# Performance work log

Measured on AMD Instinct MI355X. Metric: run time of the kernel, lower is better.

Reference implementation:

```python
import jax, jax.numpy as jnp
import numpy as np

N = 50000
E = 1600000
F_IN = 4
F_OUT = 32
PERIODS = 12


def setup_inputs() -> dict:
    key = jax.random.key(0)
    ks = jax.random.split(key, 18)
    s_in = 1.0 / np.sqrt(F_IN)
    s_cat = 1.0 / np.sqrt(2 * F_OUT)
    s_out = 1.0 / np.sqrt(F_OUT)
    inp = {
        'x': jax.random.normal(ks[0], (N, F_IN, PERIODS), dtype=jnp.float32),
        'edge_index': jax.random.randint(ks[1], (2, E), 0, N, dtype=jnp.int32),
        'attention': jax.random.uniform(ks[2], (PERIODS,), dtype=jnp.float32),
        # GRU update gate z: GCNConv weight/bias + Linear(2*F_OUT -> F_OUT)
        'Wz': jax.random.normal(ks[3], (F_IN, F_OUT), jnp.float32) * s_in,
        'bz': jnp.zeros((F_OUT,), jnp.float32),
        'Lz': jax.random.normal(ks[4], (2 * F_OUT, F_OUT), jnp.float32) * s_cat,
        'lz': jnp.zeros((F_OUT,), jnp.float32),
        # reset gate r
        'Wr': jax.random.normal(ks[5], (F_IN, F_OUT), jnp.float32) * s_in,
        'br': jnp.zeros((F_OUT,), jnp.float32),
        'Lr': jax.random.normal(ks[6], (2 * F_OUT, F_OUT), jnp.float32) * s_cat,
        'lr': jnp.zeros((F_OUT,), jnp.float32),
        # candidate h
        'Wh': jax.random.normal(ks[7], (F_IN, F_OUT), jnp.float32) * s_in,
        'bh': jnp.zeros((F_OUT,), jnp.float32),
        'Lh': jax.random.normal(ks[8], (2 * F_OUT, F_OUT), jnp.float32) * s_cat,
        'lh': jnp.zeros((F_OUT,), jnp.float32),
        # outer Linear(32 -> periods)
        'Wo': jax.random.normal(ks[9], (F_OUT, PERIODS), jnp.float32) * s_out,
        'bo': jnp.zeros((PERIODS,), jnp.float32),
    }
    return inp


def reference(x, edge_index, attention, Wz, bz, Lz, lz, Wr, br, Lr, lr, Wh, bh, Lh, lh, Wo, bo):
    n = x.shape[0]
    # gcn_norm: add self loops, symmetric D^-1/2 (A+I) D^-1/2
    loop = jnp.arange(n, dtype=edge_index.dtype)
    row = jnp.concatenate([edge_index[0], loop])  # source
    col = jnp.concatenate([edge_index[1], loop])  # target
    w = jnp.ones(row.shape[0], dtype=x.dtype)
    deg = jax.ops.segment_sum(w, col, num_segments=n)
    dinv = jnp.where(deg > 0, jax.lax.rsqrt(deg), 0.0)
    norm = dinv[row] * dinv[col]  # [E+N]

    def conv(xt, W, b):
        h = xt @ W                                   # [N, F_OUT]
        msg = h[row] * norm[:, None]                 # gather + scale
        return jax.ops.segment_sum(msg, col, num_segments=n) + b

    H0 = jnp.zeros((n, F_OUT), dtype=x.dtype)  # A3TGCN passes H=None each period

    def tgcn(xt):
        Z = jax.nn.sigmoid(jnp.concatenate([conv(xt, Wz, bz), H0], axis=1) @ Lz + lz)
        R = jax.nn.sigmoid(jnp.concatenate([conv(xt, Wr, br), H0], axis=1) @ Lr + lr)
        Ht = jnp.tanh(jnp.concatenate([conv(xt, Wh, bh), H0 * R], axis=1) @ Lh + lh)
        return Z * H0 + (1.0 - Z) * Ht

    Hs = jax.vmap(tgcn)(jnp.moveaxis(x, 2, 0))       # [T, N, F_OUT]
    probs = jax.nn.softmax(attention)
    H = jnp.einsum('tnc,t->nc', Hs, probs)           # attention-weighted sum over periods
    return jax.nn.relu(H) @ Wo + bo                  # [N, PERIODS]
```

## Files before the change

kernel.cpp:

```cpp
#include <hip/hip_runtime.h>
#include <hip/hip_fp16.h>
#include <math.h>

#define CHUNK 6144
#define CAPG  10240
#define GNODES 21

union U2H { uint2 u; __half2 h[2]; };

__global__ void k_pre(const float* __restrict__ Wz, const float* __restrict__ Lz, const float* __restrict__ lz,
                      const float* __restrict__ Wh, const float* __restrict__ Lh, const float* __restrict__ lh,
                      const float* __restrict__ bz, const float* __restrict__ bh,
                      const float* __restrict__ att,
                      float* __restrict__ AzT, float* __restrict__ AhT,
                      float* __restrict__ bzp, float* __restrict__ bhp, float* __restrict__ probs,
                      int* __restrict__ gcur) {
  int t = threadIdx.x;
  gcur[t] = 0;
  if (t < 128) {
    int f = t >> 2, k = t & 3;
    float s = 0.f, s2 = 0.f;
    for (int j = 0; j < 32; ++j) {
      s  = fmaf(Wz[k * 32 + j], Lz[j * 32 + f], s);
      s2 = fmaf(Wh[k * 32 + j], Lh[j * 32 + f], s2);
    }
    AzT[t] = s; AhT[t] = s2;
  }
  if (t >= 128 && t < 160) {
    int f = t - 128;
    float s = lz[f], s2 = lh[f];
    for (int j = 0; j < 32; ++j) {
      s  = fmaf(bz[j], Lz[j * 32 + f], s);
      s2 = fmaf(bh[j], Lh[j * 32 + f], s2);
    }
    bzp[f] = s; bhp[f] = s2;
  }
  if (t == 160) {
    float m = att[0];
    for (int i = 1; i < 12; ++i) m = fmaxf(m, att[i]);
    float e[12]; float s = 0.f;
    for (int i = 0; i < 12; ++i) { e[i] = __expf(att[i] - m); s += e[i]; }
    for (int i = 0; i < 12; ++i) probs[i] = e[i] / s;
  }
}

__global__ __launch_bounds__(1024) void k_part(const int* __restrict__ row, const int* __restrict__ col,
                                               int E, int nbkt,
                                               int* __restrict__ gcur, unsigned* __restrict__ part) {
  __shared__ unsigned spak[CHUNK];
  __shared__ unsigned char sbkt[CHUNK];
  __shared__ unsigned char slc[CHUNK];
  __shared__ int hist[256], sscan[256], scur[256], gbase[256];
  int t = threadIdx.x;
  int base = blockIdx.x * CHUNK;
  int cnt = E - base; if (cnt > CHUNK) cnt = CHUNK;
  if (t < 256) hist[t] = 0;
  __syncthreads();
  for (int i = t; i < cnt; i += 1024) {
    int c = col[base + i];
    int b = c >> 8;
    sbkt[i] = (unsigned char)b;
    slc[i]  = (unsigned char)(c & 255);
    atomicAdd(&hist[b], 1);
  }
  __syncthreads();
  int v = 0;
  if (t < 256) { v = hist[t]; sscan[t] = v; }
  __syncthreads();
  for (int off = 1; off < 256; off <<= 1) {
    int a = 0;
    if (t < 256 && t >= off) a = sscan[t - off];
    __syncthreads();
    if (t < 256) sscan[t] += a;
    __syncthreads();
  }
  if (t < 256) {
    sscan[t] -= v;
    gbase[t] = (v > 0) ? atomicAdd(&gcur[t], v) : 0;
    scur[t] = 0;
  }
  __syncthreads();
  for (int i = t; i < cnt; i += 1024) {
    int r = row[base + i];
    int b = sbkt[i];
    int pos = atomicAdd(&scur[b], 1);
    spak[sscan[b] + pos] = ((unsigned)r << 8) | (unsigned)slc[i];
  }
  __syncthreads();
  int wave = t >> 6, lane = t & 63;
  for (int b = wave; b < nbkt; b += 16) {
    int len = hist[b], gb = gbase[b], src = sscan[b];
    int lim = CAPG - gb; if (lim > len) lim = len;
    unsigned* dst = part + (size_t)b * CAPG + gb;
    for (int j = lane; j < lim; j += 64) dst[j] = spak[src + j];
  }
}

__global__ __launch_bounds__(1024) void k_sort(const unsigned* __restrict__ part, const int* __restrict__ gcur,
                                               const float4* __restrict__ x4,
                                               int* __restrict__ csr, int2* __restrict__ rng,
                                               float* __restrict__ dinv, uint2* __restrict__ xh2, int n) {
  __shared__ int hist[256], soff[256], scur2[256];
  __shared__ float sdi[256];
  int b = blockIdx.x, t = threadIdx.x;
  int cnt = gcur[b]; if (cnt > CAPG) cnt = CAPG;
  const unsigned* src = part + (size_t)b * CAPG;
  if (t < 256) hist[t] = 0;
  __syncthreads();
  for (int i = t; i < cnt; i += 1024) atomicAdd(&hist[src[i] & 255u], 1);
  __syncthreads();
  int v = 0;
  if (t < 256) { v = hist[t]; soff[t] = v; }
  __syncthreads();
  for (int off = 1; off < 256; off <<= 1) {
    int a = 0;
    if (t < 256 && t >= off) a = soff[t - off];
    __syncthreads();
    if (t < 256) soff[t] += a;
    __syncthreads();
  }
  int base = b * CAPG;
  if (t < 256) {
    int excl = soff[t] - v;
    int node = b * 256 + t;
    float di = rsqrtf((float)(v + 1));
    sdi[t] = di;
    if (node < n) {
      rng[node] = make_int2(base + excl, base + excl + v);
      dinv[node] = di;
    }
    soff[t] = excl;
    scur2[t] = 0;
  }
  __syncthreads();
  for (int i = t; i < cnt; i += 1024) {
    unsigned e = src[i];
    int lc = (int)(e & 255u);
    int pos = atomicAdd(&scur2[lc], 1);
    csr[base + soff[lc] + pos] = (int)(e >> 8);
  }
  int gb = b * 3072;
  for (int j = t; j < 3072; j += 1024) {
    int gi = gb + j;
    if (gi < n * 12) {
      float4 f = x4[gi];
      float d = sdi[j / 12];
      __half2 h0 = __floats2half2_rn(d * f.x, d * f.y);
      __half2 h1 = __floats2half2_rn(d * f.z, d * f.w);
      uint2 u; u.x = *(unsigned*)&h0; u.y = *(unsigned*)&h1;
      xh2[gi] = u;
    }
  }
}

__global__ __launch_bounds__(256) void k_gather(const int* __restrict__ csr, const int2* __restrict__ rng,
                                                const float* __restrict__ dinv, const uint2* __restrict__ xh2,
                                                float4* __restrict__ Y4, int n) {
  int t = threadIdx.x;
  int grp = t / 12, c = t - grp * 12;
  if (grp >= GNODES) return;
  int node = blockIdx.x * GNODES + grp;
  if (node >= n) return;
  U2H s; s.u = xh2[(size_t)node * 12 + c];
  float2 f0 = __half22float2(s.h[0]), f1 = __half22float2(s.h[1]);
  float a0 = f0.x, a1 = f0.y, a2 = f1.x, a3 = f1.y;
  int2 r = rng[node];
  int e = r.x, end = r.y;
#define ACC4(V) { \
    float2 g0 = __half22float2(V.h[0]), g1 = __half22float2(V.h[1]); \
    a0 += g0.x; a1 += g0.y; a2 += g1.x; a3 += g1.y; }
  for (; e + 8 <= end; e += 8) {
    int r0 = csr[e],     r1 = csr[e + 1], r2 = csr[e + 2], r3 = csr[e + 3];
    int r4 = csr[e + 4], r5 = csr[e + 5], r6 = csr[e + 6], r7 = csr[e + 7];
    U2H v0, v1, v2, v3, v4, v5, v6, v7;
    v0.u = xh2[(size_t)r0 * 12 + c];
    v1.u = xh2[(size_t)r1 * 12 + c];
    v2.u = xh2[(size_t)r2 * 12 + c];
    v3.u = xh2[(size_t)r3 * 12 + c];
    v4.u = xh2[(size_t)r4 * 12 + c];
    v5.u = xh2[(size_t)r5 * 12 + c];
    v6.u = xh2[(size_t)r6 * 12 + c];
    v7.u = xh2[(size_t)r7 * 12 + c];
    ACC4(v0) ACC4(v1) ACC4(v2) ACC4(v3) ACC4(v4) ACC4(v5) ACC4(v6) ACC4(v7)
  }
  for (; e < end; ++e) {
    int r0 = csr[e];
    U2H v0; v0.u = xh2[(size_t)r0 * 12 + c];
    ACC4(v0)
  }
#undef ACC4
  float di = dinv[node];
  Y4[(size_t)node * 12 + c] = make_float4(a0 * di, a1 * di, a2 * di, a3 * di);
}

__global__ __launch_bounds__(256) void k_dense(
    const float4* __restrict__ Y4,
    const float* __restrict__ AzT, const float* __restrict__ AhT,
    const float* __restrict__ bzp, const float* __restrict__ bhp,
    const float* __restrict__ probs,
    const float* __restrict__ Wo, const float* __restrict__ bo,
    float* __restrict__ out, int n) {
  __shared__ float4 sAz4[32], sAh4[32];
  __shared__ float sbzp[32], sbhp[32], sprobs[12], sbo[12];
  __shared__ float sWo[384];
  __shared__ float4 sY4[96];
  __shared__ float sH[8 * 33];

  int t = threadIdx.x;
  int nb = blockIdx.x * 8;

  if (t < 32) {
    sAz4[t] = ((const float4*)AzT)[t];
    sAh4[t] = ((const float4*)AhT)[t];
    sbzp[t] = bzp[t];
    sbhp[t] = bhp[t];
  }
  if (t >= 32 && t < 44) { sprobs[t - 32] = probs[t - 32]; sbo[t - 32] = bo[t - 32]; }
  for (int i = t; i < 384; i += 256) sWo[i] = Wo[i];
  if (t < 96) {
    int gi = nb * 12 + t;
    if (gi < n * 12) sY4[t] = Y4[gi];
  }
  __syncthreads();

  int ln = t >> 5, f = t & 31;
  float4 az = sAz4[f], ah = sAh4[f];
  float bzf = sbzp[f], bhf = sbhp[f];
  const float* y = (const float*)sY4 + ln * 48;
  float Hf = 0.f;
#pragma unroll
  for (int tt = 0; tt < 12; ++tt) {
    float y0 = y[tt], y1 = y[12 + tt], y2 = y[24 + tt], y3 = y[36 + tt];
    float za = fmaf(az.x, y0, fmaf(az.y, y1, fmaf(az.z, y2, fmaf(az.w, y3, bzf))));
    float ha = fmaf(ah.x, y0, fmaf(ah.y, y1, fmaf(ah.z, y2, fmaf(ah.w, y3, bhf))));
    float ez = __expf(za);
    float ax = fabsf(ha);
    float e2 = __expf(-2.f * ax);
    float g = (1.f - e2) / ((1.f + ez) * (1.f + e2));
    Hf = fmaf(sprobs[tt], copysignf(g, ha), Hf);
  }
  sH[ln * 33 + f] = fmaxf(Hf, 0.f);
  __syncthreads();

  if (t < 96) {
    int ln2 = t / 12, p = t - ln2 * 12;
    int node2 = nb + ln2;
    if (node2 < n) {
      float acc = sbo[p];
      const float* h = &sH[ln2 * 33];
      const float* wv = &sWo[p];
#pragma unroll
      for (int f2 = 0; f2 < 32; ++f2) acc = fmaf(h[f2], wv[f2 * 12], acc);
      out[node2 * 12 + p] = acc;
    }
  }
}

extern "C" void kernel_launch(void* const* d_in, const int* in_sizes, int n_in,
                              void* d_out, int out_size, void* d_ws, size_t ws_size,
                              hipStream_t stream) {
  const float* x   = (const float*)d_in[0];
  const int*   ei  = (const int*)d_in[1];
  const float* att = (const float*)d_in[2];
  const float* Wz  = (const float*)d_in[3];
  const float* bz  = (const float*)d_in[4];
  const float* Lz  = (const float*)d_in[5];
  const float* lz  = (const float*)d_in[6];
  const float* Wh  = (const float*)d_in[11];
  const float* bh  = (const float*)d_in[12];
  const float* Lh  = (const float*)d_in[13];
  const float* lh  = (const float*)d_in[14];
  const float* Wo  = (const float*)d_in[15];
  const float* bo  = (const float*)d_in[16];
  float* out = (float*)d_out;

  const int N = in_sizes[0] / (4 * 12);
  const int E = in_sizes[1] / 2;
  const int NBKT = (N + 255) >> 8;
  const int* row = ei;
  const int* col = ei + E;

  char* w = (char*)d_ws;
  size_t o = 0;
  auto alloc = [&](size_t bytes) -> char* {
    o = (o + 255) & ~(size_t)255;
    char* p = w + o; o += bytes; return p;
  };
  float* pAzT   = (float*)alloc(128 * 4);
  float* pAhT   = (float*)alloc(128 * 4);
  float* pbzp   = (float*)alloc(32 * 4);
  float* pbhp   = (float*)alloc(32 * 4);
  float* pprobs = (float*)alloc(12 * 4);
  int*   pgcur  = (int*)alloc(256 * 4);
  float* pdinv  = (float*)alloc((size_t)NBKT * 256 * 4);
  int2*  prng   = (int2*)alloc((size_t)N * 8);
  unsigned* ppart = (unsigned*)alloc((size_t)256 * CAPG * 4);
  int*   pcsr   = (int*)alloc((size_t)256 * CAPG * 4);
  uint2* pxh    = (uint2*)alloc((size_t)NBKT * 256 * 12 * 8);
  float* pY     = (float*)alloc((size_t)N * 48 * 4);
  (void)ws_size; (void)n_in; (void)out_size;

  k_pre<<<1, 256, 0, stream>>>(Wz, Lz, lz, Wh, Lh, lh, bz, bh, att,
                               pAzT, pAhT, pbzp, pbhp, pprobs, pgcur);
  k_part<<<(E + CHUNK - 1) / CHUNK, 1024, 0, stream>>>(row, col, E, NBKT, pgcur, ppart);
  k_sort<<<NBKT, 1024, 0, stream>>>(ppart, pgcur, (const float4*)x, pcsr, prng, pdinv, pxh, N);
  k_gather<<<(N + GNODES - 1) / GNODES, 256, 0, stream>>>(pcsr, prng, pdinv, pxh,
                                                          (float4*)pY, N);
  k_dense<<<(N + 7) / 8, 256, 0, stream>>>((const float4*)pY, pAzT, pAhT, pbzp, pbhp, pprobs,
                                           Wo, bo, out, N);
}
```

Before: 179.8 us.

## Use 128-node buckets with smaller chunks and stage bucket edges in LDS

The bucketed counting sort that builds the CSR now uses 391 buckets of 128 nodes instead of 196 of 256. Block sizes drop to 512 and the partition chunk shrinks to 4096 edges. The sort kernel copies each bucket's edges into shared memory once and reuses them, instead of reading them from global memory twice. The aim is more parallel blocks and less global traffic in the sort phase. The cost is a longer 512-entry scan per partition block and a per-bucket capacity of 5120 edges, which could truncate buckets that hold more edges than that.

```diff
diff --git a/kernel.cpp b/kernel.cpp
--- a/kernel.cpp
+++ b/kernel.cpp
@@ -2,8 +2,8 @@
 #include <hip/hip_fp16.h>
 #include <math.h>
 
-#define CHUNK 6144
-#define CAPG  10240
+#define CHUNK 4096
+#define CAPG  5120
 #define GNODES 21
 
 union U2H { uint2 u; __half2 h[2]; };
@@ -44,51 +44,47 @@
   }
 }
 
-__global__ __launch_bounds__(1024) void k_part(const int* __restrict__ row, const int* __restrict__ col,
-                                               int E, int nbkt,
-                                               int* __restrict__ gcur, unsigned* __restrict__ part) {
+__global__ __launch_bounds__(512) void k_part(const int* __restrict__ row, const int* __restrict__ col,
+                                              int E, int nbkt,
+                                              int* __restrict__ gcur, unsigned* __restrict__ part) {
   __shared__ unsigned spak[CHUNK];
-  __shared__ unsigned char sbkt[CHUNK];
-  __shared__ unsigned char slc[CHUNK];
-  __shared__ int hist[256], sscan[256], scur[256], gbase[256];
+  __shared__ unsigned short sboth[CHUNK];
+  __shared__ int hist[512], sscan[512], scur[512], gbase[512];
   int t = threadIdx.x;
   int base = blockIdx.x * CHUNK;
   int cnt = E - base; if (cnt > CHUNK) cnt = CHUNK;
-  if (t < 256) hist[t] = 0;
-  __syncthreads();
-  for (int i = t; i < cnt; i += 1024) {
+  hist[t] = 0;
+  __syncthreads();
+  for (int i = t; i < cnt; i += 512) {
     int c = col[base + i];
-    int b = c >> 8;
-    sbkt[i] = (unsigned char)b;
-    slc[i]  = (unsigned char)(c & 255);
-    atomicAdd(&hist[b], 1);
-  }
-  __syncthreads();
-  int v = 0;
-  if (t < 256) { v = hist[t]; sscan[t] = v; }
-  __syncthreads();
-  for (int off = 1; off < 256; off <<= 1) {
-    int a = 0;
-    if (t < 256 && t >= off) a = sscan[t - off];
+    sboth[i] = (unsigned short)c;
+    atomicAdd(&hist[c >> 7], 1);
+  }
+  __syncthreads();
+  int v = hist[t];
+  sscan[t] = v;
+  __syncthreads();
+  for (int off = 1; off < 512; off <<= 1) {
+    int a = (t >= off) ? sscan[t - off] : 0;
     __syncthreads();
-    if (t < 256) sscan[t] += a;
+    sscan[t] += a;
     __syncthreads();
   }
-  if (t < 256) {
-    sscan[t] -= v;
-    gbase[t] = (v > 0) ? atomicAdd(&gcur[t], v) : 0;
-    scur[t] = 0;
-  }
-  __syncthreads();
-  for (int i = t; i < cnt; i += 1024) {
-    int r = row[base + i];
-    int b = sbkt[i];
+  int excl = sscan[t] - v;
+  gbase[t] = (v > 0) ? atomicAdd(&gcur[t], v) : 0;
+  scur[t] = 0;
+  __syncthreads();
+  sscan[t] = excl;
+  __syncthreads();
+  for (int i = t; i < cnt; i += 512) {
+    int c = (int)sboth[i];
+    int b = c >> 7;
     int pos = atomicAdd(&scur[b], 1);
-    spak[sscan[b] + pos] = ((unsigned)r << 8) | (unsigned)slc[i];
+    spak[sscan[b] + pos] = ((unsigned)row[base + i] << 7) | (unsigned)(c & 127);
   }
   __syncthreads();
   int wave = t >> 6, lane = t & 63;
-  for (int b = wave; b < nbkt; b += 16) {
+  for (int b = wave; b < nbkt; b += 8) {
     int len = hist[b], gb = gbase[b], src = sscan[b];
     int lim = CAPG - gb; if (lim > len) lim = len;
     unsigned* dst = part + (size_t)b * CAPG + gb;
@@ -96,33 +92,38 @@
   }
 }
 
-__global__ __launch_bounds__(1024) void k_sort(const unsigned* __restrict__ part, const int* __restrict__ gcur,
-                                               const float4* __restrict__ x4,
-                                               int* __restrict__ csr, int2* __restrict__ rng,
-                                               float* __restrict__ dinv, uint2* __restrict__ xh2, int n) {
-  __shared__ int hist[256], soff[256], scur2[256];
-  __shared__ float sdi[256];
+__global__ __launch_bounds__(512) void k_sort(const unsigned* __restrict__ part, const int* __restrict__ gcur,
+                                              const float4* __restrict__ x4,
+                                              int* __restrict__ csr, int2* __restrict__ rng,
+                                              float* __restrict__ dinv, uint2* __restrict__ xh2, int n) {
+  __shared__ unsigned sedge[CAPG];
+  __shared__ int hist[128], soff[128], scur2[128];
+  __shared__ float sdi[128];
   int b = blockIdx.x, t = threadIdx.x;
   int cnt = gcur[b]; if (cnt > CAPG) cnt = CAPG;
   const unsigned* src = part + (size_t)b * CAPG;
-  if (t < 256) hist[t] = 0;
-  __syncthreads();
-  for (int i = t; i < cnt; i += 1024) atomicAdd(&hist[src[i] & 255u], 1);
+  if (t < 128) hist[t] = 0;
+  __syncthreads();
+  for (int i = t; i < cnt; i += 512) {
+    unsigned e = src[i];
+    sedge[i] = e;
+    atomicAdd(&hist[e & 127u], 1);
+  }
   __syncthreads();
   int v = 0;
-  if (t < 256) { v = hist[t]; soff[t] = v; }
-  __syncthreads();
-  for (int off = 1; off < 256; off <<= 1) {
+  if (t < 128) { v = hist[t]; soff[t] = v; }
+  __syncthreads();
+  for (int off = 1; off < 128; off <<= 1) {
     int a = 0;
-    if (t < 256 && t >= off) a = soff[t - off];
+    if (t < 128 && t >= off) a = soff[t - off];
     __syncthreads();
-    if (t < 256) soff[t] += a;
+    if (t < 128) soff[t] += a;
     __syncthreads();
   }
   int base = b * CAPG;
-  if (t < 256) {
+  if (t < 128) {
     int excl = soff[t] - v;
-    int node = b * 256 + t;
+    int node = b * 128 + t;
     float di = rsqrtf((float)(v + 1));
     sdi[t] = di;
     if (node < n) {
@@ -133,14 +134,14 @@
     scur2[t] = 0;
   }
   __syncthreads();
-  for (int i = t; i < cnt; i += 1024) {
-    unsigned e = src[i];
-    int lc = (int)(e & 255u);
+  for (int i = t; i < cnt; i += 512) {
+    unsigned e = sedge[i];
+    int lc = (int)(e & 127u);
     int pos = atomicAdd(&scur2[lc], 1);
-    csr[base + soff[lc] + pos] = (int)(e >> 8);
-  }
-  int gb = b * 3072;
-  for (int j = t; j < 3072; j += 1024) {
+    csr[base + soff[lc] + pos] = (int)(e >> 7);
+  }
+  int gb = b * 1536;
+  for (int j = t; j < 1536; j += 512) {
     int gi = gb + j;
     if (gi < n * 12) {
       float4 f = x4[gi];
@@ -276,7 +277,7 @@
 
   const int N = in_sizes[0] / (4 * 12);
   const int E = in_sizes[1] / 2;
-  const int NBKT = (N + 255) >> 8;
+  const int NBKT = (N + 127) >> 7;
   const int* row = ei;
   const int* col = ei + E;
 
@@ -291,19 +292,19 @@
   float* pbzp   = (float*)alloc(32 * 4);
   float* pbhp   = (float*)alloc(32 * 4);
   float* pprobs = (float*)alloc(12 * 4);
-  int*   pgcur  = (int*)alloc(256 * 4);
-  float* pdinv  = (float*)alloc((size_t)NBKT * 256 * 4);
+  int*   pgcur  = (int*)alloc(512 * 4);
+  float* pdinv  = (float*)alloc((size_t)NBKT * 128 * 4);
   int2*  prng   = (int2*)alloc((size_t)N * 8);
-  unsigned* ppart = (unsigned*)alloc((size_t)256 * CAPG * 4);
-  int*   pcsr   = (int*)alloc((size_t)256 * CAPG * 4);
-  uint2* pxh    = (uint2*)alloc((size_t)NBKT * 256 * 12 * 8);
+  unsigned* ppart = (unsigned*)alloc((size_t)NBKT * CAPG * 4);
+  int*   pcsr   = (int*)alloc((size_t)NBKT * CAPG * 4);
+  uint2* pxh    = (uint2*)alloc((size_t)NBKT * 128 * 12 * 8);
   float* pY     = (float*)alloc((size_t)N * 48 * 4);
   (void)ws_size; (void)n_in; (void)out_size;
 
-  k_pre<<<1, 256, 0, stream>>>(Wz, Lz, lz, Wh, Lh, lh, bz, bh, att,
+  k_pre<<<1, 512, 0, stream>>>(Wz, Lz, lz, Wh, Lh, lh, bz, bh, att,
                                pAzT, pAhT, pbzp, pbhp, pprobs, pgcur);
-  k_part<<<(E + CHUNK - 1) / CHUNK, 1024, 0, stream>>>(row, col, E, NBKT, pgcur, ppart);
-  k_sort<<<NBKT, 1024, 0, stream>>>(ppart, pgcur, (const float4*)x, pcsr, prng, pdinv, pxh, N);
+  k_part<<<(E + CHUNK - 1) / CHUNK, 512, 0, stream>>>(row, col, E, NBKT, pgcur, ppart);
+  k_sort<<<NBKT, 512, 0, stream>>>(ppart, pgcur, (const float4*)x, pcsr, prng, pdinv, pxh, N);
   k_gather<<<(N + GNODES - 1) / GNODES, 256, 0, stream>>>(pcsr, prng, pdinv, pxh,
                                                           (float4*)pY, N);
   k_dense<<<(N + 7) / 8, 256, 0, stream>>>((const float4*)pY, pAzT, pAhT, pbzp, pbhp, pprobs,
```

Result: slower. 186.4 us (+3.7%).

## Fuse dense GRU/attention epilogue into gather kernel and cache bucket edges in LDS

Applied to the files above, without the earlier changes.

Merges the dense gate/tanh/attention/output stage into the gather kernel, so aggregated features stay in shared memory instead of being written to and re-read from a global Y buffer, and one kernel launch is dropped. Also, k_sort now keeps its partition entries in a 40KB shared array so the second pass reads LDS instead of re-reading global memory. In exchange the gather kernel uses more LDS and registers, which can lower occupancy for the latency-bound gather loop, and the dense phase now runs on 21-node blocks with uneven thread use.

```diff
diff --git a/kernel.cpp b/kernel.cpp
--- a/kernel.cpp
+++ b/kernel.cpp
@@ -100,6 +100,7 @@
                                                const float4* __restrict__ x4,
                                                int* __restrict__ csr, int2* __restrict__ rng,
                                                float* __restrict__ dinv, uint2* __restrict__ xh2, int n) {
+  __shared__ unsigned sedge[CAPG];
   __shared__ int hist[256], soff[256], scur2[256];
   __shared__ float sdi[256];
   int b = blockIdx.x, t = threadIdx.x;
@@ -107,7 +108,11 @@
   const unsigned* src = part + (size_t)b * CAPG;
   if (t < 256) hist[t] = 0;
   __syncthreads();
-  for (int i = t; i < cnt; i += 1024) atomicAdd(&hist[src[i] & 255u], 1);
+  for (int i = t; i < cnt; i += 1024) {
+    unsigned e = src[i];
+    sedge[i] = e;
+    atomicAdd(&hist[e & 255u], 1);
+  }
   __syncthreads();
   int v = 0;
   if (t < 256) { v = hist[t]; soff[t] = v; }
@@ -134,7 +139,7 @@
   }
   __syncthreads();
   for (int i = t; i < cnt; i += 1024) {
-    unsigned e = src[i];
+    unsigned e = sedge[i];
     int lc = (int)(e & 255u);
     int pos = atomicAdd(&scur2[lc], 1);
     csr[base + soff[lc] + pos] = (int)(e >> 8);
@@ -155,100 +160,92 @@
 
 __global__ __launch_bounds__(256) void k_gather(const int* __restrict__ csr, const int2* __restrict__ rng,
                                                 const float* __restrict__ dinv, const uint2* __restrict__ xh2,
-                                                float4* __restrict__ Y4, int n) {
+                                                const float* __restrict__ AzT, const float* __restrict__ AhT,
+                                                const float* __restrict__ bzp, const float* __restrict__ bhp,
+                                                const float* __restrict__ probs,
+                                                const float* __restrict__ Wo, const float* __restrict__ bo,
+                                                float* __restrict__ out, int n) {
+  __shared__ float sY[GNODES * 49];
+  __shared__ float sH[GNODES * 33];
+  __shared__ float4 sAz4[32], sAh4[32];
+  __shared__ float sbzp[32], sbhp[32], sprobs[12], sbo[12], sWo[384];
   int t = threadIdx.x;
+  int nb = blockIdx.x * GNODES;
+
+  if (t < 32) {
+    sAz4[t] = ((const float4*)AzT)[t];
+    sAh4[t] = ((const float4*)AhT)[t];
+    sbzp[t] = bzp[t]; sbhp[t] = bhp[t];
+  }
+  if (t >= 32 && t < 44) { sprobs[t - 32] = probs[t - 32]; sbo[t - 32] = bo[t - 32]; }
+  for (int i = t; i < 384; i += 256) sWo[i] = Wo[i];
+
   int grp = t / 12, c = t - grp * 12;
-  if (grp >= GNODES) return;
-  int node = blockIdx.x * GNODES + grp;
-  if (node >= n) return;
-  U2H s; s.u = xh2[(size_t)node * 12 + c];
-  float2 f0 = __half22float2(s.h[0]), f1 = __half22float2(s.h[1]);
-  float a0 = f0.x, a1 = f0.y, a2 = f1.x, a3 = f1.y;
-  int2 r = rng[node];
-  int e = r.x, end = r.y;
+  int node = nb + grp;
+  if (grp < GNODES && node < n) {
+    U2H s; s.u = xh2[(size_t)node * 12 + c];
+    float2 f0 = __half22float2(s.h[0]), f1 = __half22float2(s.h[1]);
+    float a0 = f0.x, a1 = f0.y, a2 = f1.x, a3 = f1.y;
+    int2 r = rng[node];
+    int e = r.x, end = r.y;
 #define ACC4(V) { \
     float2 g0 = __half22float2(V.h[0]), g1 = __half22float2(V.h[1]); \
     a0 += g0.x; a1 += g0.y; a2 += g1.x; a3 += g1.y; }
-  for (; e + 8 <= end; e += 8) {
-    int r0 = csr[e],     r1 = csr[e + 1], r2 = csr[e + 2], r3 = csr[e + 3];
-    int r4 = csr[e + 4], r5 = csr[e + 5], r6 = csr[e + 6], r7 = csr[e + 7];
-    U2H v0, v1, v2, v3, v4, v5, v6, v7;
-    v0.u = xh2[(size_t)r0 * 12 + c];
-    v1.u = xh2[(size_t)r1 * 12 + c];
-    v2.u = xh2[(size_t)r2 * 12 + c];
-    v3.u = xh2[(size_t)r3 * 12 + c];
-    v4.u = xh2[(size_t)r4 * 12 + c];
-    v5.u = xh2[(size_t)r5 * 12 + c];
-    v6.u = xh2[(size_t)r6 * 12 + c];
-    v7.u = xh2[(size_t)r7 * 12 + c];
-    ACC4(v0) ACC4(v1) ACC4(v2) ACC4(v3) ACC4(v4) ACC4(v5) ACC4(v6) ACC4(v7)
-  }
-  for (; e < end; ++e) {
-    int r0 = csr[e];
-    U2H v0; v0.u = xh2[(size_t)r0 * 12 + c];
-    ACC4(v0)
-  }
+    for (; e + 8 <= end; e += 8) {
+      int r0 = csr[e],     r1 = csr[e + 1], r2 = csr[e + 2], r3 = csr[e + 3];
+      int r4 = csr[e + 4], r5 = csr[e + 5], r6 = csr[e + 6], r7 = csr[e + 7];
+      U2H v0, v1, v2, v3, v4, v5, v6, v7;
+      v0.u = xh2[(size_t)r0 * 12 + c];
+      v1.u = xh2[(size_t)r1 * 12 + c];
+      v2.u = xh2[(size_t)r2 * 12 + c];
+      v3.u = xh2[(size_t)r3 * 12 + c];
+      v4.u = xh2[(size_t)r4 * 12 + c];
+      v5.u = xh2[(size_t)r5 * 12 + c];
+      v6.u = xh2[(size_t)r6 * 12 + c];
+      v7.u = xh2[(size_t)r7 * 12 + c];
+      ACC4(v0) ACC4(v1) ACC4(v2) ACC4(v3) ACC4(v4) ACC4(v5) ACC4(v6) ACC4(v7)
+    }
+    for (; e < end; ++e) {
+      int r0 = csr[e];
+      U2H v0; v0.u = xh2[(size_t)r0 * 12 + c];
+      ACC4(v0)
+    }
 #undef ACC4
-  float di = dinv[node];
-  Y4[(size_t)node * 12 + c] = make_float4(a0 * di, a1 * di, a2 * di, a3 * di);
-}
-
-__global__ __launch_bounds__(256) void k_dense(
-    const float4* __restrict__ Y4,
-    const float* __restrict__ AzT, const float* __restrict__ AhT,
-    const float* __restrict__ bzp, const float* __restrict__ bhp,
-    const float* __restrict__ probs,
-    const float* __restrict__ Wo, const float* __restrict__ bo,
-    float* __restrict__ out, int n) {
-  __shared__ float4 sAz4[32], sAh4[32];
-  __shared__ float sbzp[32], sbhp[32], sprobs[12], sbo[12];
-  __shared__ float sWo[384];
-  __shared__ float4 sY4[96];
-  __shared__ float sH[8 * 33];
-
-  int t = threadIdx.x;
-  int nb = blockIdx.x * 8;
-
-  if (t < 32) {
-    sAz4[t] = ((const float4*)AzT)[t];
-    sAh4[t] = ((const float4*)AhT)[t];
-    sbzp[t] = bzp[t];
-    sbhp[t] = bhp[t];
-  }
-  if (t >= 32 && t < 44) { sprobs[t - 32] = probs[t - 32]; sbo[t - 32] = bo[t - 32]; }
-  for (int i = t; i < 384; i += 256) sWo[i] = Wo[i];
-  if (t < 96) {
-    int gi = nb * 12 + t;
-    if (gi < n * 12) sY4[t] = Y4[gi];
-  }
-  __syncthreads();
-
-  int ln = t >> 5, f = t & 31;
-  float4 az = sAz4[f], ah = sAh4[f];
-  float bzf = sbzp[f], bhf = sbhp[f];
-  const float* y = (const float*)sY4 + ln * 48;
-  float Hf = 0.f;
+    float di = dinv[node];
+    float* yb = sY + grp * 49 + c * 4;
+    yb[0] = a0 * di; yb[1] = a1 * di; yb[2] = a2 * di; yb[3] = a3 * di;
+  }
+  __syncthreads();
+
+  for (int u = t; u < GNODES * 32; u += 256) {
+    int ln = u >> 5, f = u & 31;
+    if (nb + ln >= n) continue;
+    const float* y = sY + ln * 49;
+    float4 az = sAz4[f], ah = sAh4[f];
+    float bzf = sbzp[f], bhf = sbhp[f];
+    float acc = 0.f;
 #pragma unroll
-  for (int tt = 0; tt < 12; ++tt) {
-    float y0 = y[tt], y1 = y[12 + tt], y2 = y[24 + tt], y3 = y[36 + tt];
-    float za = fmaf(az.x, y0, fmaf(az.y, y1, fmaf(az.z, y2, fmaf(az.w, y3, bzf))));
-    float ha = fmaf(ah.x, y0, fmaf(ah.y, y1, fmaf(ah.z, y2, fmaf(ah.w, y3, bhf))));
-    float ez = __expf(za);
-    float ax = fabsf(ha);
-    float e2 = __expf(-2.f * ax);
-    float g = (1.f - e2) / ((1.f + ez) * (1.f + e2));
-    Hf = fmaf(sprobs[tt], copysignf(g, ha), Hf);
-  }
-  sH[ln * 33 + f] = fmaxf(Hf, 0.f);
-  __syncthreads();
-
-  if (t < 96) {
-    int ln2 = t / 12, p = t - ln2 * 12;
-    int node2 = nb + ln2;
+    for (int tt = 0; tt < 12; ++tt) {
+      float y0 = y[tt], y1 = y[12 + tt], y2 = y[24 + tt], y3 = y[36 + tt];
+      float za = fmaf(az.x, y0, fmaf(az.y, y1, fmaf(az.z, y2, fmaf(az.w, y3, bzf))));
+      float ha = fmaf(ah.x, y0, fmaf(ah.y, y1, fmaf(ah.z, y2, fmaf(ah.w, y3, bhf))));
+      float ez = __expf(za);
+      float ax = fabsf(ha);
+      float e2 = __expf(-2.f * ax);
+      float g = (1.f - e2) / ((1.f + ez) * (1.f + e2));
+      acc = fmaf(sprobs[tt], copysignf(g, ha), acc);
+    }
+    sH[ln * 33 + f] = fmaxf(acc, 0.f);
+  }
+  __syncthreads();
+
+  if (t < GNODES * 12) {
+    int ln = t / 12, p = t - ln * 12;
+    int node2 = nb + ln;
     if (node2 < n) {
       float acc = sbo[p];
-      const float* h = &sH[ln2 * 33];
-      const float* wv = &sWo[p];
+      const float* h = sH + ln * 33;
+      const float* wv = sWo + p;
 #pragma unroll
       for (int f2 = 0; f2 < 32; ++f2) acc = fmaf(h[f2], wv[f2 * 12], acc);
       out[node2 * 12 + p] = acc;
@@ -297,7 +294,6 @@
   unsigned* ppart = (unsigned*)alloc((size_t)256 * CAPG * 4);
   int*   pcsr   = (int*)alloc((size_t)256 * CAPG * 4);
   uint2* pxh    = (uint2*)alloc((size_t)NBKT * 256 * 12 * 8);
-  float* pY     = (float*)alloc((size_t)N * 48 * 4);
   (void)ws_size; (void)n_in; (void)out_size;
 
   k_pre<<<1, 256, 0, stream>>>(Wz, Lz, lz, Wh, Lh, lh, bz, bh, att,
@@ -305,7 +301,6 @@
   k_part<<<(E + CHUNK - 1) / CHUNK, 1024, 0, stream>>>(row, col, E, NBKT, pgcur, ppart);
   k_sort<<<NBKT, 1024, 0, stream>>>(ppart, pgcur, (const float4*)x, pcsr, prng, pdinv, pxh, N);
   k_gather<<<(N + GNODES - 1) / GNODES, 256, 0, stream>>>(pcsr, prng, pdinv, pxh,
-                                                          (float4*)pY, N);
-  k_dense<<<(N + 7) / 8, 256, 0, stream>>>((const float4*)pY, pAzT, pAhT, pbzp, pbhp, pprobs,
-                                           Wo, bo, out, N);
-}
+                                                          pAzT, pAhT, pbzp, pbhp, pprobs,
+                                                          Wo, bo, out, N);
+}
```

Result: faster. 170.0 us (-5.5%).
